# Kernel optimization log

Measured on AMD Instinct MI355X. Metric: run time of the kernel, lower is better.

The kernel has to match this reference:

```python
import jax, jax.numpy as jnp
import numpy as np

N_ELEC = 64
IN_C = 64
HID = [64, 128]
OUT_C = 128
BATCH = 2048
BN_EPS = 1e-5


def build_graph():
    """Replicates EEGGraphNet._build_graph_structure with random 3D electrode positions."""
    rng = np.random.RandomState(0)
    pos = rng.rand(N_ELEC, 3).astype(np.float64)
    d = np.sqrt(((pos[:, None, :] - pos[None, :, :]) ** 2).sum(-1))
    thr = np.percentile(d[d > 0], 30)
    src, dst = [], []
    for i in range(N_ELEC):
        for j in range(i + 1, N_ELEC):
            if d[i, j] < thr:
                src += [i, j]
                dst += [j, i]
    return np.asarray(src, np.int32), np.asarray(dst, np.int32)


def setup_inputs() -> dict:
    key = jax.random.key(0)
    ks = jax.random.split(key, 8)
    src, dst = build_graph()
    dims = [IN_C] + HID + [OUT_C]  # [64, 64, 128, 128]
    inp = {"x": jax.random.normal(ks[0], (BATCH, N_ELEC, IN_C), jnp.float32)}
    for li in range(3):
        fi, fo = dims[li], dims[li + 1]
        inp[f"W{li+1}"] = jax.random.normal(ks[li + 1], (fi, fo), jnp.float32) * (1.0 / np.sqrt(fi))
        inp[f"b{li+1}"] = jnp.zeros((fo,), jnp.float32)
    for li in range(2):  # BN after first two convs
        inp[f"g{li+1}"] = jnp.ones((dims[li + 1],), jnp.float32)
        inp[f"be{li+1}"] = jnp.zeros((dims[li + 1],), jnp.float32)
    inp["src"] = jnp.asarray(src)
    inp["dst"] = jnp.asarray(dst)
    return inp


def gcn_conv(x, W, b, src, dst, edge_norm, self_norm):
    # x: (B, N, Fin) -> (B, N, Fout). GCN with self-loops, symmetric norm.
    h = jnp.einsum("bnf,fo->bno", x, W)
    msg = h[:, src, :] * edge_norm[None, :, None]          # (B, E, Fout) gather
    agg = jnp.zeros_like(h).at[:, dst, :].add(msg)         # scatter-add over dst
    return agg + h * self_norm[None, :, None] + b


def batchnorm(x, g, be):
    # torch BatchNorm1d over flattened (B*N, C) nodes, training-mode batch stats
    m = jnp.mean(x, axis=(0, 1))
    v = jnp.mean((x - m) ** 2, axis=(0, 1))
    return g * (x - m) * jax.lax.rsqrt(v + BN_EPS) + be


def reference(x, W1, b1, W2, b2, W3, b3, g1, be1, g2, be2, src, dst):
    # degree (with self-loop) is identical across graphs in the batch
    deg = jnp.zeros((N_ELEC,), x.dtype).at[dst].add(1.0) + 1.0
    inv_sqrt = jax.lax.rsqrt(deg)
    edge_norm = inv_sqrt[src] * inv_sqrt[dst]
    self_norm = 1.0 / deg

    h = gcn_conv(x, W1, b1, src, dst, edge_norm, self_norm)
    h = jax.nn.relu(batchnorm(h, g1, be1))
    h = gcn_conv(h, W2, b2, src, dst, edge_norm, self_norm)
    h = jax.nn.relu(batchnorm(h, g2, be2))
    h = gcn_conv(h, W3, b3, src, dst, edge_norm, self_norm)
    return jnp.mean(h, axis=1)  # global mean pool over electrodes -> (B, OUT_C)
```

## Files before the change

### kernel.cpp

```cpp
#include <hip/hip_runtime.h>
#include <hip/hip_bf16.h>

typedef unsigned short ushortT;
typedef unsigned int uintT;

#define BATCH   2048
#define NELEC   64
#define BN_EPS  1e-5f

#define OFF_A      0
#define OFF_AMEAN  4096
#define OFF_SS1    4160
#define OFF_SS2    4288
#define OFF_PS1    4544
#define OFF_PQ1    8640
#define OFF_PS2    12736
#define OFF_PQ2    20928
#define OFF_H1     29120
#define OFF_H2     (29120 + 8388608)

__device__ inline float bf2f(ushortT u) { return __uint_as_float(((uintT)u) << 16); }
__device__ inline ushortT f2bf(float f) {
  uintT u = __float_as_uint(f);
  u = (u + 0x7FFFu + ((u >> 16) & 1u)) >> 16;
  return (ushortT)u;
}

__global__ __launch_bounds__(256) void prep_kernel(const int* __restrict__ src,
                                                   const int* __restrict__ dst,
                                                   int E, float* __restrict__ ws) {
  __shared__ float degS[NELEC];
  __shared__ float As[NELEC * NELEC];
  int t = threadIdx.x;
  if (t < NELEC) degS[t] = 1.0f;
  for (int i = t; i < NELEC * NELEC; i += 256) As[i] = 0.0f;
  __syncthreads();
  for (int e = t; e < E; e += 256) atomicAdd(&degS[dst[e]], 1.0f);
  __syncthreads();
  for (int e = t; e < E; e += 256) {
    float en = rsqrtf(degS[src[e]]) * rsqrtf(degS[dst[e]]);
    atomicAdd(&As[dst[e] * NELEC + src[e]], en);
  }
  __syncthreads();
  if (t < NELEC) As[t * NELEC + t] += 1.0f / degS[t];
  __syncthreads();
  for (int i = t; i < NELEC * NELEC; i += 256) ws[OFF_A + i] = As[i];
  if (t < NELEC) {
    float s = 0.0f;
    for (int n = 0; n < NELEC; ++n) s += As[n * NELEC + t];
    ws[OFF_AMEAN + t] = s * (1.0f / NELEC);
  }
  for (int i = t; i < (OFF_H1 - OFF_PS1); i += 256) ws[OFF_PS1 + i] = 0.0f;
}

__global__ __launch_bounds__(256) void layer1_kernel(const float* __restrict__ x,
    const float* __restrict__ W1, const float* __restrict__ b1,
    float* __restrict__ ws) {
  __shared__ float Xs[64][68];
  __shared__ float Wsh[64][68];
  __shared__ float Ash[64][68];
  const int b = blockIdx.x;
  const int t = threadIdx.x;
  const int tn = t >> 4, to = t & 15;
  const int tn4 = tn * 4, to4 = to * 4;

  const float4* xb  = (const float4*)(x + (size_t)b * 4096);
  const float4* w1v = (const float4*)W1;
  const float4* av  = (const float4*)(ws + OFF_A);
  for (int i = t; i < 1024; i += 256) {
    int row = i >> 4, c = (i & 15) * 4;
    *(float4*)&Xs[row][c]  = xb[i];
    *(float4*)&Wsh[row][c] = w1v[i];
    *(float4*)&Ash[row][c] = av[i];
  }
  __syncthreads();

  float acc[4][4] = {};
  #pragma unroll 16
  for (int k = 0; k < 64; ++k) {
    float a[4];
    #pragma unroll
    for (int i = 0; i < 4; ++i) a[i] = Xs[tn4 + i][k];
    float4 bv = *(const float4*)&Wsh[k][to4];
    #pragma unroll
    for (int i = 0; i < 4; ++i) {
      acc[i][0] = fmaf(a[i], bv.x, acc[i][0]);
      acc[i][1] = fmaf(a[i], bv.y, acc[i][1]);
      acc[i][2] = fmaf(a[i], bv.z, acc[i][2]);
      acc[i][3] = fmaf(a[i], bv.w, acc[i][3]);
    }
  }
  __syncthreads();
  #pragma unroll
  for (int i = 0; i < 4; ++i)
    *(float4*)&Xs[tn4 + i][to4] = make_float4(acc[i][0], acc[i][1], acc[i][2], acc[i][3]);
  __syncthreads();

  float h[4][4] = {};
  #pragma unroll 16
  for (int m = 0; m < 64; ++m) {
    float a[4];
    #pragma unroll
    for (int i = 0; i < 4; ++i) a[i] = Ash[tn4 + i][m];
    float4 bv = *(const float4*)&Xs[m][to4];
    #pragma unroll
    for (int i = 0; i < 4; ++i) {
      h[i][0] = fmaf(a[i], bv.x, h[i][0]);
      h[i][1] = fmaf(a[i], bv.y, h[i][1]);
      h[i][2] = fmaf(a[i], bv.z, h[i][2]);
      h[i][3] = fmaf(a[i], bv.w, h[i][3]);
    }
  }
  float4 bias = ((const float4*)b1)[to];
  float psum[4] = {}, psq[4] = {};
  float* h1p = ws + OFF_H1 + (size_t)b * 4096;
  #pragma unroll
  for (int i = 0; i < 4; ++i) {
    float4 hv;
    hv.x = h[i][0] + bias.x; hv.y = h[i][1] + bias.y;
    hv.z = h[i][2] + bias.z; hv.w = h[i][3] + bias.w;
    ((float4*)(h1p + (size_t)(tn4 + i) * 64))[to] = hv;
    psum[0] += hv.x; psq[0] += hv.x * hv.x;
    psum[1] += hv.y; psq[1] += hv.y * hv.y;
    psum[2] += hv.z; psq[2] += hv.z * hv.z;
    psum[3] += hv.w; psq[3] += hv.w * hv.w;
  }
  __syncthreads();
  #pragma unroll
  for (int j = 0; j < 4; ++j) {
    Wsh[tn][to4 + j] = psum[j];
    Ash[tn][to4 + j] = psq[j];
  }
  __syncthreads();
  if (t < 64) {
    float S = 0.0f, Q = 0.0f;
    #pragma unroll
    for (int g = 0; g < 16; ++g) { S += Wsh[g][t]; Q += Ash[g][t]; }
    int slot = b & 63;
    atomicAdd(&ws[OFF_PS1 + slot * 64 + t], S);
    atomicAdd(&ws[OFF_PQ1 + slot * 64 + t], Q);
  }
}

__global__ void reduce1_kernel(const float* __restrict__ g1, const float* __restrict__ be1,
                               float* __restrict__ ws) {
  int t = threadIdx.x;
  if (t < 64) {
    float S = 0.0f, Q = 0.0f;
    for (int s = 0; s < 64; ++s) { S += ws[OFF_PS1 + s * 64 + t]; Q += ws[OFF_PQ1 + s * 64 + t]; }
    const float inv = 1.0f / (float)(BATCH * NELEC);
    float m = S * inv;
    float v = fmaxf(Q * inv - m * m, 0.0f);
    float sc = g1[t] * rsqrtf(v + BN_EPS);
    ws[OFF_SS1 + t] = sc;
    ws[OFF_SS1 + 64 + t] = fmaf(-m, sc, be1[t]);
  }
}

__global__ void reduce2_kernel(const float* __restrict__ g2, const float* __restrict__ be2,
                               float* __restrict__ ws) {
  int t = threadIdx.x;
  if (t < 128) {
    float S = 0.0f, Q = 0.0f;
    for (int s = 0; s < 64; ++s) { S += ws[OFF_PS2 + s * 128 + t]; Q += ws[OFF_PQ2 + s * 128 + t]; }
    const float inv = 1.0f / (float)(BATCH * NELEC);
    float m = S * inv;
    float v = fmaxf(Q * inv - m * m, 0.0f);
    float sc = g2[t] * rsqrtf(v + BN_EPS);
    ws[OFF_SS2 + t] = sc;
    ws[OFF_SS2 + 128 + t] = fmaf(-m, sc, be2[t]);
  }
}

__global__ __launch_bounds__(256) void layer2_kernel(const float* __restrict__ W2,
    const float* __restrict__ b2, float* __restrict__ ws) {
  __shared__ float Ys[64][68];
  __shared__ float Wsh[64][132];
  const int b = blockIdx.x, t = threadIdx.x;
  const int tn = t >> 4, to = t & 15;
  const int tn4 = tn * 4, to8 = to * 8;

  const float4* h1v  = (const float4*)(ws + OFF_H1 + (size_t)b * 4096);
  const float4* s1v  = (const float4*)(ws + OFF_SS1);
  const float4* sh1v = (const float4*)(ws + OFF_SS1 + 64);
  for (int i = t; i < 1024; i += 256) {
    int c4 = i & 15;
    float4 v = h1v[i];
    float4 s = s1v[c4], sh = sh1v[c4];
    v.x = fmaxf(fmaf(v.x, s.x, sh.x), 0.0f);
    v.y = fmaxf(fmaf(v.y, s.y, sh.y), 0.0f);
    v.z = fmaxf(fmaf(v.z, s.z, sh.z), 0.0f);
    v.w = fmaxf(fmaf(v.w, s.w, sh.w), 0.0f);
    *(float4*)&Ys[i >> 4][c4 * 4] = v;
  }
  const float4* w2v = (const float4*)W2;
  for (int i = t; i < 2048; i += 256)
    *(float4*)&Wsh[i >> 5][(i & 31) * 4] = w2v[i];
  __syncthreads();

  float acc[4][8] = {};
  #pragma unroll 8
  for (int k = 0; k < 64; ++k) {
    float a[4];
    #pragma unroll
    for (int i = 0; i < 4; ++i) a[i] = Ys[tn4 + i][k];
    float4 b0 = *(const float4*)&Wsh[k][to8];
    float4 b1v = *(const float4*)&Wsh[k][to8 + 4];
    #pragma unroll
    for (int i = 0; i < 4; ++i) {
      acc[i][0] = fmaf(a[i], b0.x, acc[i][0]);
      acc[i][1] = fmaf(a[i], b0.y, acc[i][1]);
      acc[i][2] = fmaf(a[i], b0.z, acc[i][2]);
      acc[i][3] = fmaf(a[i], b0.w, acc[i][3]);
      acc[i][4] = fmaf(a[i], b1v.x, acc[i][4]);
      acc[i][5] = fmaf(a[i], b1v.y, acc[i][5]);
      acc[i][6] = fmaf(a[i], b1v.z, acc[i][6]);
      acc[i][7] = fmaf(a[i], b1v.w, acc[i][7]);
    }
  }
  __syncthreads();
  #pragma unroll
  for (int i = 0; i < 4; ++i) {
    *(float4*)&Wsh[tn4 + i][to8]     = make_float4(acc[i][0], acc[i][1], acc[i][2], acc[i][3]);
    *(float4*)&Wsh[tn4 + i][to8 + 4] = make_float4(acc[i][4], acc[i][5], acc[i][6], acc[i][7]);
  }
  const float4* av = (const float4*)(ws + OFF_A);
  for (int i = t; i < 1024; i += 256)
    *(float4*)&Ys[i >> 4][(i & 15) * 4] = av[i];
  __syncthreads();

  float h[4][8] = {};
  #pragma unroll 8
  for (int m = 0; m < 64; ++m) {
    float a[4];
    #pragma unroll
    for (int i = 0; i < 4; ++i) a[i] = Ys[tn4 + i][m];
    float4 b0 = *(const float4*)&Wsh[m][to8];
    float4 b1v = *(const float4*)&Wsh[m][to8 + 4];
    #pragma unroll
    for (int i = 0; i < 4; ++i) {
      h[i][0] = fmaf(a[i], b0.x, h[i][0]);
      h[i][1] = fmaf(a[i], b0.y, h[i][1]);
      h[i][2] = fmaf(a[i], b0.z, h[i][2]);
      h[i][3] = fmaf(a[i], b0.w, h[i][3]);
      h[i][4] = fmaf(a[i], b1v.x, h[i][4]);
      h[i][5] = fmaf(a[i], b1v.y, h[i][5]);
      h[i][6] = fmaf(a[i], b1v.z, h[i][6]);
      h[i][7] = fmaf(a[i], b1v.w, h[i][7]);
    }
  }
  float4 bias0 = ((const float4*)b2)[to * 2];
  float4 bias1 = ((const float4*)b2)[to * 2 + 1];
  float psum[8] = {}, psq[8] = {};
  ushortT* h2p = (ushortT*)(ws + OFF_H2) + (size_t)b * 8192;
  #pragma unroll
  for (int i = 0; i < 4; ++i) {
    float v[8];
    v[0] = h[i][0] + bias0.x; v[1] = h[i][1] + bias0.y;
    v[2] = h[i][2] + bias0.z; v[3] = h[i][3] + bias0.w;
    v[4] = h[i][4] + bias1.x; v[5] = h[i][5] + bias1.y;
    v[6] = h[i][6] + bias1.z; v[7] = h[i][7] + bias1.w;
    uint4 pk;
    pk.x = (uintT)f2bf(v[0]) | ((uintT)f2bf(v[1]) << 16);
    pk.y = (uintT)f2bf(v[2]) | ((uintT)f2bf(v[3]) << 16);
    pk.z = (uintT)f2bf(v[4]) | ((uintT)f2bf(v[5]) << 16);
    pk.w = (uintT)f2bf(v[6]) | ((uintT)f2bf(v[7]) << 16);
    *(uint4*)(h2p + (size_t)(tn4 + i) * 128 + to8) = pk;
    #pragma unroll
    for (int j = 0; j < 8; ++j) { psum[j] += v[j]; psq[j] += v[j] * v[j]; }
  }
  __syncthreads();
  float* red = &Ys[0][0];
  #pragma unroll
  for (int j = 0; j < 8; ++j) {
    red[tn * 128 + to8 + j] = psum[j];
    red[2048 + tn * 128 + to8 + j] = psq[j];
  }
  __syncthreads();
  if (t < 128) {
    float S = 0.0f, Q = 0.0f;
    #pragma unroll
    for (int g = 0; g < 16; ++g) { S += red[g * 128 + t]; Q += red[2048 + g * 128 + t]; }
    int slot = b & 63;
    atomicAdd(&ws[OFF_PS2 + slot * 128 + t], S);
    atomicAdd(&ws[OFF_PQ2 + slot * 128 + t], Q);
  }
}

#define L3_ITEMS 4
__global__ __launch_bounds__(256) void layer3_kernel(const float* __restrict__ W3,
    const float* __restrict__ b3, const float* __restrict__ ws,
    float* __restrict__ out) {
  __shared__ float W3s[128][132];
  __shared__ float vS[2][128];
  __shared__ float oS[128];
  __shared__ float am[64];
  const int t = threadIdx.x;
  const int g = t >> 7, f = t & 127;
  const float4* w3v = (const float4*)W3;
  for (int i = t; i < 4096; i += 256)
    *(float4*)&W3s[i >> 5][(i & 31) * 4] = w3v[i];
  if (t < 64) am[t] = ws[OFF_AMEAN + t];
  float s2  = ws[OFF_SS2 + f];
  float sh2 = ws[OFF_SS2 + 128 + f];
  float b3f = b3[f];
  __syncthreads();
  const ushortT* h2base = (const ushortT*)(ws + OFF_H2);
  for (int it = 0; it < L3_ITEMS; ++it) {
    int b = blockIdx.x * L3_ITEMS + it;
    const ushortT* h2b = h2base + (size_t)b * 8192;
    float vp = 0.0f;
    #pragma unroll 8
    for (int m = g; m < 64; m += 2) {
      float hv = bf2f(h2b[m * 128 + f]);
      vp += am[m] * fmaxf(fmaf(hv, s2, sh2), 0.0f);
    }
    vS[g][f] = vp;
    __syncthreads();
    float acc = 0.0f;
    #pragma unroll 8
    for (int k = 0; k < 64; ++k) {
      int fk = (g << 6) + k;
      acc = fmaf(vS[0][fk] + vS[1][fk], W3s[fk][f], acc);
    }
    if (g == 0) oS[f] = acc;
    __syncthreads();
    if (g == 1) out[(size_t)b * 128 + f] = oS[f] + acc + b3f;
    __syncthreads();
  }
}

extern "C" void kernel_launch(void* const* d_in, const int* in_sizes, int n_in,
                              void* d_out, int out_size, void* d_ws, size_t ws_size,
                              hipStream_t stream) {
  const float* x   = (const float*)d_in[0];
  const float* W1  = (const float*)d_in[1];
  const float* b1  = (const float*)d_in[2];
  const float* W2  = (const float*)d_in[3];
  const float* b2  = (const float*)d_in[4];
  const float* W3  = (const float*)d_in[5];
  const float* b3  = (const float*)d_in[6];
  const float* g1  = (const float*)d_in[7];
  const float* be1 = (const float*)d_in[8];
  const float* g2  = (const float*)d_in[9];
  const float* be2 = (const float*)d_in[10];
  const int*   src = (const int*)d_in[11];
  const int*   dst = (const int*)d_in[12];
  const int E = in_sizes[11];
  float* ws  = (float*)d_ws;
  float* out = (float*)d_out;

  hipLaunchKernelGGL(prep_kernel,   dim3(1),              dim3(256), 0, stream, src, dst, E, ws);
  hipLaunchKernelGGL(layer1_kernel, dim3(BATCH),          dim3(256), 0, stream, x, W1, b1, ws);
  hipLaunchKernelGGL(reduce1_kernel,dim3(1),              dim3(64),  0, stream, g1, be1, ws);
  hipLaunchKernelGGL(layer2_kernel, dim3(BATCH),          dim3(256), 0, stream, W2, b2, ws);
  hipLaunchKernelGGL(reduce2_kernel,dim3(1),              dim3(128), 0, stream, g2, be2, ws);
  hipLaunchKernelGGL(layer3_kernel, dim3(BATCH/L3_ITEMS), dim3(256), 0, stream, W3, b3, ws, out);
}
```

Before: 218.0 us.

## Rewrite GCN layers with split-bf16 MFMA and bf16 intermediate storage

Layers 1 and 2 are rewritten to run on bf16 MFMA (16x16x32), with one wave per graph. Operands are split into hi/lo bf16 pairs and combined with three MFMAs to keep near-fp32 accuracy, and the weights and adjacency are pre-split and transposed in the prep kernel. H1 is now stored as bf16, which halves its traffic, and layer3 is rewritten as one wave per item using shuffles instead of shared-memory W3. The aim is to replace the scalar FP32 FMA work with matrix cores and cut memory traffic, in exchange for the extra MFMAs from the split and some rounding error in the intermediates.

New measurement: 200.9 us. 7.9% less time.

```diff
diff --git a/kernel.cpp b/kernel.cpp
--- a/kernel.cpp
+++ b/kernel.cpp
@@ -3,12 +3,13 @@
 
 typedef unsigned short ushortT;
 typedef unsigned int uintT;
+typedef __attribute__((ext_vector_type(8))) short short8;
+typedef __attribute__((ext_vector_type(4))) float f32x4;
 
 #define BATCH   2048
 #define NELEC   64
 #define BN_EPS  1e-5f
 
-#define OFF_A      0
 #define OFF_AMEAN  4096
 #define OFF_SS1    4160
 #define OFF_SS2    4288
@@ -16,8 +17,13 @@
 #define OFF_PQ1    8640
 #define OFF_PS2    12736
 #define OFF_PQ2    20928
-#define OFF_H1     29120
-#define OFF_H2     (29120 + 8388608)
+#define OFF_ABF    29120
+#define OFF_W1T    33216
+#define OFF_W2T    37312
+#define OFF_H1     45504
+#define OFF_H2     4239808
+
+#define MFMA(a, b, c) __builtin_amdgcn_mfma_f32_16x16x32_bf16(a, b, c, 0, 0, 0)
 
 __device__ inline float bf2f(ushortT u) { return __uint_as_float(((uintT)u) << 16); }
 __device__ inline ushortT f2bf(float f) {
@@ -25,10 +31,23 @@
   u = (u + 0x7FFFu + ((u >> 16) & 1u)) >> 16;
   return (ushortT)u;
 }
+__device__ inline void split2(float f, ushortT& hi, ushortT& lo) {
+  hi = f2bf(f);
+  lo = f2bf(f - bf2f(hi));
+}
+__device__ inline void split8(const float* f, short8& hi, short8& lo) {
+  #pragma unroll
+  for (int e = 0; e < 8; ++e) {
+    ushortT h, l;
+    split2(f[e], h, l);
+    hi[e] = (short)h; lo[e] = (short)l;
+  }
+}
 
 __global__ __launch_bounds__(256) void prep_kernel(const int* __restrict__ src,
-                                                   const int* __restrict__ dst,
-                                                   int E, float* __restrict__ ws) {
+    const int* __restrict__ dst, int E,
+    const float* __restrict__ W1, const float* __restrict__ W2,
+    float* __restrict__ ws) {
   __shared__ float degS[NELEC];
   __shared__ float As[NELEC * NELEC];
   int t = threadIdx.x;
@@ -44,101 +63,113 @@
   __syncthreads();
   if (t < NELEC) As[t * NELEC + t] += 1.0f / degS[t];
   __syncthreads();
-  for (int i = t; i < NELEC * NELEC; i += 256) ws[OFF_A + i] = As[i];
+  ushortT* abf = (ushortT*)(ws + OFF_ABF);
+  for (int i = t; i < 4096; i += 256) {
+    ushortT hi, lo; split2(As[i], hi, lo);
+    abf[i] = hi; abf[4096 + i] = lo;
+  }
   if (t < NELEC) {
     float s = 0.0f;
     for (int n = 0; n < NELEC; ++n) s += As[n * NELEC + t];
     ws[OFF_AMEAN + t] = s * (1.0f / NELEC);
   }
-  for (int i = t; i < (OFF_H1 - OFF_PS1); i += 256) ws[OFF_PS1 + i] = 0.0f;
-}
-
-__global__ __launch_bounds__(256) void layer1_kernel(const float* __restrict__ x,
-    const float* __restrict__ W1, const float* __restrict__ b1,
-    float* __restrict__ ws) {
-  __shared__ float Xs[64][68];
-  __shared__ float Wsh[64][68];
-  __shared__ float Ash[64][68];
-  const int b = blockIdx.x;
-  const int t = threadIdx.x;
-  const int tn = t >> 4, to = t & 15;
-  const int tn4 = tn * 4, to4 = to * 4;
-
-  const float4* xb  = (const float4*)(x + (size_t)b * 4096);
-  const float4* w1v = (const float4*)W1;
-  const float4* av  = (const float4*)(ws + OFF_A);
-  for (int i = t; i < 1024; i += 256) {
-    int row = i >> 4, c = (i & 15) * 4;
-    *(float4*)&Xs[row][c]  = xb[i];
-    *(float4*)&Wsh[row][c] = w1v[i];
-    *(float4*)&Ash[row][c] = av[i];
-  }
-  __syncthreads();
-
-  float acc[4][4] = {};
-  #pragma unroll 16
-  for (int k = 0; k < 64; ++k) {
-    float a[4];
-    #pragma unroll
-    for (int i = 0; i < 4; ++i) a[i] = Xs[tn4 + i][k];
-    float4 bv = *(const float4*)&Wsh[k][to4];
-    #pragma unroll
-    for (int i = 0; i < 4; ++i) {
-      acc[i][0] = fmaf(a[i], bv.x, acc[i][0]);
-      acc[i][1] = fmaf(a[i], bv.y, acc[i][1]);
-      acc[i][2] = fmaf(a[i], bv.z, acc[i][2]);
-      acc[i][3] = fmaf(a[i], bv.w, acc[i][3]);
-    }
-  }
-  __syncthreads();
+  ushortT* w1t = (ushortT*)(ws + OFF_W1T);
+  for (int i = t; i < 4096; i += 256) {
+    int o = i >> 6, k = i & 63;
+    ushortT hi, lo; split2(W1[k * 64 + o], hi, lo);
+    w1t[i] = hi; w1t[4096 + i] = lo;
+  }
+  ushortT* w2t = (ushortT*)(ws + OFF_W2T);
+  for (int i = t; i < 8192; i += 256) {
+    int o = i >> 6, k = i & 63;
+    ushortT hi, lo; split2(W2[k * 128 + o], hi, lo);
+    w2t[i] = hi; w2t[8192 + i] = lo;
+  }
+}
+
+__global__ __launch_bounds__(256) void layer1_mfma(const float* __restrict__ x,
+    const float* __restrict__ b1, float* __restrict__ ws) {
+  __shared__ ushortT TsH[4][16 * 72];
+  __shared__ ushortT TsL[4][16 * 72];
+  const int w = threadIdx.x >> 6, lane = threadIdx.x & 63;
+  const int item = blockIdx.x * 4 + w;
+  const int c = lane & 15, g = lane >> 4;
+  const ushortT* abf = (const ushortT*)(ws + OFF_ABF);
+  const ushortT* w1t = (const ushortT*)(ws + OFF_W1T);
+  ushortT* h1p = (ushortT*)(ws + OFF_H1) + (size_t)item * 4096;
+  ushortT* tsh = &TsH[w][0];
+  ushortT* tsl = &TsL[w][0];
+
+  short8 Xhi[4][2], Xlo[4][2];
   #pragma unroll
-  for (int i = 0; i < 4; ++i)
-    *(float4*)&Xs[tn4 + i][to4] = make_float4(acc[i][0], acc[i][1], acc[i][2], acc[i][3]);
-  __syncthreads();
-
-  float h[4][4] = {};
-  #pragma unroll 16
-  for (int m = 0; m < 64; ++m) {
-    float a[4];
-    #pragma unroll
-    for (int i = 0; i < 4; ++i) a[i] = Ash[tn4 + i][m];
-    float4 bv = *(const float4*)&Xs[m][to4];
-    #pragma unroll
-    for (int i = 0; i < 4; ++i) {
-      h[i][0] = fmaf(a[i], bv.x, h[i][0]);
-      h[i][1] = fmaf(a[i], bv.y, h[i][1]);
-      h[i][2] = fmaf(a[i], bv.z, h[i][2]);
-      h[i][3] = fmaf(a[i], bv.w, h[i][3]);
-    }
-  }
-  float4 bias = ((const float4*)b1)[to];
-  float psum[4] = {}, psq[4] = {};
-  float* h1p = ws + OFF_H1 + (size_t)b * 4096;
-  #pragma unroll
-  for (int i = 0; i < 4; ++i) {
-    float4 hv;
-    hv.x = h[i][0] + bias.x; hv.y = h[i][1] + bias.y;
-    hv.z = h[i][2] + bias.z; hv.w = h[i][3] + bias.w;
-    ((float4*)(h1p + (size_t)(tn4 + i) * 64))[to] = hv;
-    psum[0] += hv.x; psq[0] += hv.x * hv.x;
-    psum[1] += hv.y; psq[1] += hv.y * hv.y;
-    psum[2] += hv.z; psq[2] += hv.z * hv.z;
-    psum[3] += hv.w; psq[3] += hv.w * hv.w;
-  }
-  __syncthreads();
-  #pragma unroll
-  for (int j = 0; j < 4; ++j) {
-    Wsh[tn][to4 + j] = psum[j];
-    Ash[tn][to4 + j] = psq[j];
-  }
-  __syncthreads();
-  if (t < 64) {
+  for (int rt = 0; rt < 4; ++rt) {
+    #pragma unroll
+    for (int ks = 0; ks < 2; ++ks) {
+      const float* p = x + (size_t)item * 4096 + (rt * 16 + c) * 64 + ks * 32 + g * 8;
+      float4 fa = *(const float4*)p;
+      float4 fb = *(const float4*)(p + 4);
+      float f[8] = {fa.x, fa.y, fa.z, fa.w, fb.x, fb.y, fb.z, fb.w};
+      split8(f, Xhi[rt][ks], Xlo[rt][ks]);
+    }
+  }
+
+  for (int s = 0; s < 4; ++s) {
+    f32x4 t[4] = {{0,0,0,0},{0,0,0,0},{0,0,0,0},{0,0,0,0}};
+    #pragma unroll
+    for (int ks = 0; ks < 2; ++ks) {
+      short8 bh = *(const short8*)(w1t + (s * 16 + c) * 64 + ks * 32 + g * 8);
+      short8 bl = *(const short8*)(w1t + 4096 + (s * 16 + c) * 64 + ks * 32 + g * 8);
+      #pragma unroll
+      for (int rt = 0; rt < 4; ++rt) {
+        t[rt] = MFMA(Xhi[rt][ks], bh, t[rt]);
+        t[rt] = MFMA(Xhi[rt][ks], bl, t[rt]);
+        t[rt] = MFMA(Xlo[rt][ks], bh, t[rt]);
+      }
+    }
+    #pragma unroll
+    for (int rt = 0; rt < 4; ++rt) {
+      ushortT h0, h1_, h2_, h3, l0, l1, l2, l3;
+      split2(t[rt][0], h0, l0); split2(t[rt][1], h1_, l1);
+      split2(t[rt][2], h2_, l2); split2(t[rt][3], h3, l3);
+      uint2 wh, wl;
+      wh.x = (uintT)h0 | ((uintT)h1_ << 16); wh.y = (uintT)h2_ | ((uintT)h3 << 16);
+      wl.x = (uintT)l0 | ((uintT)l1 << 16);  wl.y = (uintT)l2 | ((uintT)l3 << 16);
+      int idx = c * 72 + rt * 16 + g * 4;
+      *(uint2*)(tsh + idx) = wh;
+      *(uint2*)(tsl + idx) = wl;
+    }
+    f32x4 hacc[4] = {{0,0,0,0},{0,0,0,0},{0,0,0,0},{0,0,0,0}};
+    #pragma unroll
+    for (int ks = 0; ks < 2; ++ks) {
+      short8 th = *(const short8*)(tsh + c * 72 + ks * 32 + g * 8);
+      short8 tl = *(const short8*)(tsl + c * 72 + ks * 32 + g * 8);
+      #pragma unroll
+      for (int rt = 0; rt < 4; ++rt) {
+        short8 ah = *(const short8*)(abf + (rt * 16 + c) * 64 + ks * 32 + g * 8);
+        short8 al = *(const short8*)(abf + 4096 + (rt * 16 + c) * 64 + ks * 32 + g * 8);
+        hacc[rt] = MFMA(ah, th, hacc[rt]);
+        hacc[rt] = MFMA(ah, tl, hacc[rt]);
+        hacc[rt] = MFMA(al, th, hacc[rt]);
+      }
+    }
+    float bias = b1[s * 16 + c];
     float S = 0.0f, Q = 0.0f;
     #pragma unroll
-    for (int g = 0; g < 16; ++g) { S += Wsh[g][t]; Q += Ash[g][t]; }
-    int slot = b & 63;
-    atomicAdd(&ws[OFF_PS1 + slot * 64 + t], S);
-    atomicAdd(&ws[OFF_PQ1 + slot * 64 + t], Q);
+    for (int rt = 0; rt < 4; ++rt) {
+      #pragma unroll
+      for (int r = 0; r < 4; ++r) {
+        float v = hacc[rt][r] + bias;
+        S += v; Q += v * v;
+        h1p[(rt * 16 + g * 4 + r) * 64 + s * 16 + c] = f2bf(v);
+      }
+    }
+    S += __shfl_xor(S, 16); S += __shfl_xor(S, 32);
+    Q += __shfl_xor(Q, 16); Q += __shfl_xor(Q, 32);
+    if (g == 0) {
+      int slot = item & 63;
+      atomicAdd(&ws[OFF_PS1 + slot * 64 + s * 16 + c], S);
+      atomicAdd(&ws[OFF_PQ1 + slot * 64 + s * 16 + c], Q);
+    }
   }
 }
 
@@ -172,162 +203,129 @@
   }
 }
 
-__global__ __launch_bounds__(256) void layer2_kernel(const float* __restrict__ W2,
-    const float* __restrict__ b2, float* __restrict__ ws) {
-  __shared__ float Ys[64][68];
-  __shared__ float Wsh[64][132];
-  const int b = blockIdx.x, t = threadIdx.x;
-  const int tn = t >> 4, to = t & 15;
-  const int tn4 = tn * 4, to8 = to * 8;
-
-  const float4* h1v  = (const float4*)(ws + OFF_H1 + (size_t)b * 4096);
-  const float4* s1v  = (const float4*)(ws + OFF_SS1);
-  const float4* sh1v = (const float4*)(ws + OFF_SS1 + 64);
-  for (int i = t; i < 1024; i += 256) {
-    int c4 = i & 15;
-    float4 v = h1v[i];
-    float4 s = s1v[c4], sh = sh1v[c4];
-    v.x = fmaxf(fmaf(v.x, s.x, sh.x), 0.0f);
-    v.y = fmaxf(fmaf(v.y, s.y, sh.y), 0.0f);
-    v.z = fmaxf(fmaf(v.z, s.z, sh.z), 0.0f);
-    v.w = fmaxf(fmaf(v.w, s.w, sh.w), 0.0f);
-    *(float4*)&Ys[i >> 4][c4 * 4] = v;
-  }
-  const float4* w2v = (const float4*)W2;
-  for (int i = t; i < 2048; i += 256)
-    *(float4*)&Wsh[i >> 5][(i & 31) * 4] = w2v[i];
-  __syncthreads();
-
-  float acc[4][8] = {};
-  #pragma unroll 8
-  for (int k = 0; k < 64; ++k) {
-    float a[4];
-    #pragma unroll
-    for (int i = 0; i < 4; ++i) a[i] = Ys[tn4 + i][k];
-    float4 b0 = *(const float4*)&Wsh[k][to8];
-    float4 b1v = *(const float4*)&Wsh[k][to8 + 4];
-    #pragma unroll
-    for (int i = 0; i < 4; ++i) {
-      acc[i][0] = fmaf(a[i], b0.x, acc[i][0]);
-      acc[i][1] = fmaf(a[i], b0.y, acc[i][1]);
-      acc[i][2] = fmaf(a[i], b0.z, acc[i][2]);
-      acc[i][3] = fmaf(a[i], b0.w, acc[i][3]);
-      acc[i][4] = fmaf(a[i], b1v.x, acc[i][4]);
-      acc[i][5] = fmaf(a[i], b1v.y, acc[i][5]);
-      acc[i][6] = fmaf(a[i], b1v.z, acc[i][6]);
-      acc[i][7] = fmaf(a[i], b1v.w, acc[i][7]);
-    }
-  }
-  __syncthreads();
+__global__ __launch_bounds__(256) void layer2_mfma(const float* __restrict__ b2,
+    float* __restrict__ ws) {
+  __shared__ ushortT TsH[4][16 * 72];
+  __shared__ ushortT TsL[4][16 * 72];
+  const int w = threadIdx.x >> 6, lane = threadIdx.x & 63;
+  const int item = blockIdx.x * 4 + w;
+  const int c = lane & 15, g = lane >> 4;
+  const ushortT* abf = (const ushortT*)(ws + OFF_ABF);
+  const ushortT* w2t = (const ushortT*)(ws + OFF_W2T);
+  const ushortT* h1p = (const ushortT*)(ws + OFF_H1) + (size_t)item * 4096;
+  ushortT* h2p = (ushortT*)(ws + OFF_H2) + (size_t)item * 8192;
+  ushortT* tsh = &TsH[w][0];
+  ushortT* tsl = &TsL[w][0];
+
+  short8 Yhi[4][2], Ylo[4][2];
   #pragma unroll
-  for (int i = 0; i < 4; ++i) {
-    *(float4*)&Wsh[tn4 + i][to8]     = make_float4(acc[i][0], acc[i][1], acc[i][2], acc[i][3]);
-    *(float4*)&Wsh[tn4 + i][to8 + 4] = make_float4(acc[i][4], acc[i][5], acc[i][6], acc[i][7]);
-  }
-  const float4* av = (const float4*)(ws + OFF_A);
-  for (int i = t; i < 1024; i += 256)
-    *(float4*)&Ys[i >> 4][(i & 15) * 4] = av[i];
-  __syncthreads();
-
-  float h[4][8] = {};
-  #pragma unroll 8
-  for (int m = 0; m < 64; ++m) {
-    float a[4];
-    #pragma unroll
-    for (int i = 0; i < 4; ++i) a[i] = Ys[tn4 + i][m];
-    float4 b0 = *(const float4*)&Wsh[m][to8];
-    float4 b1v = *(const float4*)&Wsh[m][to8 + 4];
-    #pragma unroll
-    for (int i = 0; i < 4; ++i) {
-      h[i][0] = fmaf(a[i], b0.x, h[i][0]);
-      h[i][1] = fmaf(a[i], b0.y, h[i][1]);
-      h[i][2] = fmaf(a[i], b0.z, h[i][2]);
-      h[i][3] = fmaf(a[i], b0.w, h[i][3]);
-      h[i][4] = fmaf(a[i], b1v.x, h[i][4]);
-      h[i][5] = fmaf(a[i], b1v.y, h[i][5]);
-      h[i][6] = fmaf(a[i], b1v.z, h[i][6]);
-      h[i][7] = fmaf(a[i], b1v.w, h[i][7]);
-    }
-  }
-  float4 bias0 = ((const float4*)b2)[to * 2];
-  float4 bias1 = ((const float4*)b2)[to * 2 + 1];
-  float psum[8] = {}, psq[8] = {};
-  ushortT* h2p = (ushortT*)(ws + OFF_H2) + (size_t)b * 8192;
-  #pragma unroll
-  for (int i = 0; i < 4; ++i) {
-    float v[8];
-    v[0] = h[i][0] + bias0.x; v[1] = h[i][1] + bias0.y;
-    v[2] = h[i][2] + bias0.z; v[3] = h[i][3] + bias0.w;
-    v[4] = h[i][4] + bias1.x; v[5] = h[i][5] + bias1.y;
-    v[6] = h[i][6] + bias1.z; v[7] = h[i][7] + bias1.w;
-    uint4 pk;
-    pk.x = (uintT)f2bf(v[0]) | ((uintT)f2bf(v[1]) << 16);
-    pk.y = (uintT)f2bf(v[2]) | ((uintT)f2bf(v[3]) << 16);
-    pk.z = (uintT)f2bf(v[4]) | ((uintT)f2bf(v[5]) << 16);
-    pk.w = (uintT)f2bf(v[6]) | ((uintT)f2bf(v[7]) << 16);
-    *(uint4*)(h2p + (size_t)(tn4 + i) * 128 + to8) = pk;
-    #pragma unroll
-    for (int j = 0; j < 8; ++j) { psum[j] += v[j]; psq[j] += v[j] * v[j]; }
-  }
-  __syncthreads();
-  float* red = &Ys[0][0];
-  #pragma unroll
-  for (int j = 0; j < 8; ++j) {
-    red[tn * 128 + to8 + j] = psum[j];
-    red[2048 + tn * 128 + to8 + j] = psq[j];
-  }
-  __syncthreads();
-  if (t < 128) {
+  for (int ks = 0; ks < 2; ++ks) {
+    const float* sp = ws + OFF_SS1 + ks * 32 + g * 8;
+    const float* tp = ws + OFF_SS1 + 64 + ks * 32 + g * 8;
+    float4 sa = *(const float4*)sp, sb = *(const float4*)(sp + 4);
+    float4 ta = *(const float4*)tp, tb = *(const float4*)(tp + 4);
+    float s8[8] = {sa.x, sa.y, sa.z, sa.w, sb.x, sb.y, sb.z, sb.w};
+    float t8[8] = {ta.x, ta.y, ta.z, ta.w, tb.x, tb.y, tb.z, tb.w};
+    #pragma unroll
+    for (int rt = 0; rt < 4; ++rt) {
+      short8 hv = *(const short8*)(h1p + (rt * 16 + c) * 64 + ks * 32 + g * 8);
+      float f[8];
+      #pragma unroll
+      for (int e = 0; e < 8; ++e)
+        f[e] = fmaxf(fmaf(bf2f((ushortT)hv[e]), s8[e], t8[e]), 0.0f);
+      split8(f, Yhi[rt][ks], Ylo[rt][ks]);
+    }
+  }
+
+  for (int s = 0; s < 8; ++s) {
+    f32x4 t[4] = {{0,0,0,0},{0,0,0,0},{0,0,0,0},{0,0,0,0}};
+    #pragma unroll
+    for (int ks = 0; ks < 2; ++ks) {
+      short8 bh = *(const short8*)(w2t + (s * 16 + c) * 64 + ks * 32 + g * 8);
+      short8 bl = *(const short8*)(w2t + 8192 + (s * 16 + c) * 64 + ks * 32 + g * 8);
+      #pragma unroll
+      for (int rt = 0; rt < 4; ++rt) {
+        t[rt] = MFMA(Yhi[rt][ks], bh, t[rt]);
+        t[rt] = MFMA(Yhi[rt][ks], bl, t[rt]);
+        t[rt] = MFMA(Ylo[rt][ks], bh, t[rt]);
+      }
+    }
+    #pragma unroll
+    for (int rt = 0; rt < 4; ++rt) {
+      ushortT h0, h1_, h2_, h3, l0, l1, l2, l3;
+      split2(t[rt][0], h0, l0); split2(t[rt][1], h1_, l1);
+      split2(t[rt][2], h2_, l2); split2(t[rt][3], h3, l3);
+      uint2 wh, wl;
+      wh.x = (uintT)h0 | ((uintT)h1_ << 16); wh.y = (uintT)h2_ | ((uintT)h3 << 16);
+      wl.x = (uintT)l0 | ((uintT)l1 << 16);  wl.y = (uintT)l2 | ((uintT)l3 << 16);
+      int idx = c * 72 + rt * 16 + g * 4;
+      *(uint2*)(tsh + idx) = wh;
+      *(uint2*)(tsl + idx) = wl;
+    }
+    f32x4 hacc[4] = {{0,0,0,0},{0,0,0,0},{0,0,0,0},{0,0,0,0}};
+    #pragma unroll
+    for (int ks = 0; ks < 2; ++ks) {
+      short8 th = *(const short8*)(tsh + c * 72 + ks * 32 + g * 8);
+      short8 tl = *(const short8*)(tsl + c * 72 + ks * 32 + g * 8);
+      #pragma unroll
+      for (int rt = 0; rt < 4; ++rt) {
+        short8 ah = *(const short8*)(abf + (rt * 16 + c) * 64 + ks * 32 + g * 8);
+        short8 al = *(const short8*)(abf + 4096 + (rt * 16 + c) * 64 + ks * 32 + g * 8);
+        hacc[rt] = MFMA(ah, th, hacc[rt]);
+        hacc[rt] = MFMA(ah, tl, hacc[rt]);
+        hacc[rt] = MFMA(al, th, hacc[rt]);
+      }
+    }
+    float bias = b2[s * 16 + c];
     float S = 0.0f, Q = 0.0f;
     #pragma unroll
-    for (int g = 0; g < 16; ++g) { S += red[g * 128 + t]; Q += red[2048 + g * 128 + t]; }
-    int slot = b & 63;
-    atomicAdd(&ws[OFF_PS2 + slot * 128 + t], S);
-    atomicAdd(&ws[OFF_PQ2 + slot * 128 + t], Q);
-  }
-}
-
-#define L3_ITEMS 4
+    for (int rt = 0; rt < 4; ++rt) {
+      #pragma unroll
+      for (int r = 0; r < 4; ++r) {
+        float v = hacc[rt][r] + bias;
+        S += v; Q += v * v;
+        h2p[(rt * 16 + g * 4 + r) * 128 + s * 16 + c] = f2bf(v);
+      }
+    }
+    S += __shfl_xor(S, 16); S += __shfl_xor(S, 32);
+    Q += __shfl_xor(Q, 16); Q += __shfl_xor(Q, 32);
+    if (g == 0) {
+      int slot = item & 63;
+      atomicAdd(&ws[OFF_PS2 + slot * 128 + s * 16 + c], S);
+      atomicAdd(&ws[OFF_PQ2 + slot * 128 + s * 16 + c], Q);
+    }
+  }
+}
+
 __global__ __launch_bounds__(256) void layer3_kernel(const float* __restrict__ W3,
     const float* __restrict__ b3, const float* __restrict__ ws,
     float* __restrict__ out) {
-  __shared__ float W3s[128][132];
-  __shared__ float vS[2][128];
-  __shared__ float oS[128];
-  __shared__ float am[64];
-  const int t = threadIdx.x;
-  const int g = t >> 7, f = t & 127;
-  const float4* w3v = (const float4*)W3;
-  for (int i = t; i < 4096; i += 256)
-    *(float4*)&W3s[i >> 5][(i & 31) * 4] = w3v[i];
-  if (t < 64) am[t] = ws[OFF_AMEAN + t];
-  float s2  = ws[OFF_SS2 + f];
-  float sh2 = ws[OFF_SS2 + 128 + f];
-  float b3f = b3[f];
-  __syncthreads();
-  const ushortT* h2base = (const ushortT*)(ws + OFF_H2);
-  for (int it = 0; it < L3_ITEMS; ++it) {
-    int b = blockIdx.x * L3_ITEMS + it;
-    const ushortT* h2b = h2base + (size_t)b * 8192;
-    float vp = 0.0f;
-    #pragma unroll 8
-    for (int m = g; m < 64; m += 2) {
-      float hv = bf2f(h2b[m * 128 + f]);
-      vp += am[m] * fmaxf(fmaf(hv, s2, sh2), 0.0f);
-    }
-    vS[g][f] = vp;
-    __syncthreads();
-    float acc = 0.0f;
-    #pragma unroll 8
-    for (int k = 0; k < 64; ++k) {
-      int fk = (g << 6) + k;
-      acc = fmaf(vS[0][fk] + vS[1][fk], W3s[fk][f], acc);
-    }
-    if (g == 0) oS[f] = acc;
-    __syncthreads();
-    if (g == 1) out[(size_t)b * 128 + f] = oS[f] + acc + b3f;
-    __syncthreads();
-  }
+  const int w = threadIdx.x >> 6, lane = threadIdx.x & 63;
+  const int item = blockIdx.x * 4 + w;
+  const int f0 = lane * 2;
+  const float s2a = ws[OFF_SS2 + f0],       s2b = ws[OFF_SS2 + f0 + 1];
+  const float t2a = ws[OFF_SS2 + 128 + f0], t2b = ws[OFF_SS2 + 128 + f0 + 1];
+  const float* am = ws + OFF_AMEAN;
+  const ushortT* h2 = (const ushortT*)(ws + OFF_H2) + (size_t)item * 8192;
+  float v0 = 0.0f, v1 = 0.0f;
+  #pragma unroll 8
+  for (int m = 0; m < 64; ++m) {
+    uintT pk = *(const uintT*)(h2 + m * 128 + f0);
+    float y0 = fmaxf(fmaf(bf2f((ushortT)(pk & 0xffffu)), s2a, t2a), 0.0f);
+    float y1 = fmaxf(fmaf(bf2f((ushortT)(pk >> 16)),     s2b, t2b), 0.0f);
+    float a = am[m];
+    v0 = fmaf(a, y0, v0);
+    v1 = fmaf(a, y1, v1);
+  }
+  float o0 = b3[f0], o1 = b3[f0 + 1];
+  #pragma unroll 8
+  for (int k = 0; k < 128; ++k) {
+    float vk = __shfl((k & 1) ? v1 : v0, k >> 1, 64);
+    o0 = fmaf(vk, W3[k * 128 + f0],     o0);
+    o1 = fmaf(vk, W3[k * 128 + f0 + 1], o1);
+  }
+  float2 ov; ov.x = o0; ov.y = o1;
+  *(float2*)(out + (size_t)item * 128 + f0) = ov;
 }
 
 extern "C" void kernel_launch(void* const* d_in, const int* in_sizes, int n_in,
@@ -350,10 +348,11 @@
   float* ws  = (float*)d_ws;
   float* out = (float*)d_out;
 
-  hipLaunchKernelGGL(prep_kernel,   dim3(1),              dim3(256), 0, stream, src, dst, E, ws);
-  hipLaunchKernelGGL(layer1_kernel, dim3(BATCH),          dim3(256), 0, stream, x, W1, b1, ws);
-  hipLaunchKernelGGL(reduce1_kernel,dim3(1),              dim3(64),  0, stream, g1, be1, ws);
-  hipLaunchKernelGGL(layer2_kernel, dim3(BATCH),          dim3(256), 0, stream, W2, b2, ws);
-  hipLaunchKernelGGL(reduce2_kernel,dim3(1),              dim3(128), 0, stream, g2, be2, ws);
-  hipLaunchKernelGGL(layer3_kernel, dim3(BATCH/L3_ITEMS), dim3(256), 0, stream, W3, b3, ws, out);
-}
+  hipMemsetAsync((void*)(ws + OFF_PS1), 0, (size_t)(29120 - OFF_PS1) * 4, stream);
+  hipLaunchKernelGGL(prep_kernel,   dim3(1),   dim3(256), 0, stream, src, dst, E, W1, W2, ws);
+  hipLaunchKernelGGL(layer1_mfma,   dim3(512), dim3(256), 0, stream, x, b1, ws);
+  hipLaunchKernelGGL(reduce1_kernel,dim3(1),   dim3(64),  0, stream, g1, be1, ws);
+  hipLaunchKernelGGL(layer2_mfma,   dim3(512), dim3(256), 0, stream, b2, ws);
+  hipLaunchKernelGGL(reduce2_kernel,dim3(1),   dim3(128), 0, stream, g2, be2, ws);
+  hipLaunchKernelGGL(layer3_kernel, dim3(512), dim3(256), 0, stream, W3, b3, ws, out);
+}
```
